# Kernel tuning notes

Hardware: AMD Instinct MI355X
Metric: run time of the kernel (lower is better)

## Reference

```python
import jax, jax.numpy as jnp
import numpy as np

HIDDEN, N_HEADS, HEAD_DIM, CACHE_LEN, BATCH = 4096, 32, 128, 512, 32


def setup_inputs() -> dict:
    key = jax.random.key(0)
    ks = jax.random.split(key, 7)
    s = 0.02
    return {
        "x": jax.random.normal(ks[0], (BATCH, 1, HIDDEN), jnp.float32),
        "k_cache": jax.random.normal(ks[1], (BATCH, N_HEADS, CACHE_LEN, HEAD_DIM), jnp.float32),
        "v_cache": jax.random.normal(ks[2], (BATCH, N_HEADS, CACHE_LEN, HEAD_DIM), jnp.float32),
        # torch nn.Linear weights: (out_features, in_features), y = x @ W.T
        "wq": jax.random.normal(ks[3], (N_HEADS * HEAD_DIM, HIDDEN), jnp.float32) * s,
        "wk": jax.random.normal(ks[4], (N_HEADS * HEAD_DIM, HIDDEN), jnp.float32) * s,
        "wv": jax.random.normal(ks[5], (N_HEADS * HEAD_DIM, HIDDEN), jnp.float32) * s,
        "wo": jax.random.normal(ks[6], (HIDDEN, N_HEADS * HEAD_DIM), jnp.float32) * s,
    }


def reference(x, k_cache, v_cache, wq, wk, wv, wo):
    bsz = x.shape[0]
    # projections: (b, 1, H*D) -> (b, n_heads, 1, head_dim)
    def proj(w):
        return (x @ w.T).reshape(bsz, 1, N_HEADS, HEAD_DIM).transpose(0, 2, 1, 3)
    q, k_new, v_new = proj(wq), proj(wk), proj(wv)
    scale = 1.0 / HEAD_DIM ** 0.5
    # cache attention: (b, h, 1, cache_len)
    cache_scores = jnp.einsum("bhqd,bhkd->bhqk", q, k_cache) * scale
    cache_probs = jax.nn.softmax(cache_scores, axis=-1)
    cache_out = jnp.einsum("bhqk,bhkd->bhqd", cache_probs, v_cache)
    # new-token attention: softmax over a single key (probs == 1), kept faithful
    new_scores = jnp.einsum("bhqd,bhkd->bhqk", q, k_new) * scale
    new_probs = jax.nn.softmax(new_scores, axis=-1)
    new_out = jnp.einsum("bhqk,bhkd->bhqd", new_probs, v_new)
    out = cache_out + new_out  # note: sum of two separately-normalized softmaxes (as in source)
    out = out.transpose(0, 2, 1, 3).reshape(bsz, 1, N_HEADS * HEAD_DIM)
    return out @ wo.T
```

## Files before the change

kernel.cpp:

```cpp
#include <hip/hip_runtime.h>
#include <hip/hip_bf16.h>

#define HIDDEN 4096
#define NHEADS 32
#define HDIM 128
#define CLEN 512
#define BATCH 32
#define KB 256

typedef float f32x4 __attribute__((ext_vector_type(4)));

__device__ __forceinline__ void proj_body(const float* __restrict__ X,
                                          const float* __restrict__ W,
                                          float* __restrict__ Y,
                                          int rowblock) {
    const int t   = threadIdx.x;
    const int l   = t & 63;
    const int wid = t >> 6;
    const int rowbase = rowblock * 8;
    const float* wp = W + (size_t)rowbase * HIDDEN + 4 * l;
    const float* xp = X + (size_t)(wid * 4) * HIDDEN + 4 * l;

    float v[32];
    #pragma unroll
    for (int j = 0; j < 32; ++j) v[j] = 0.f;

    #pragma unroll 2
    for (int kp = 0; kp < HIDDEN; kp += 256) {
        float4 wv[8], xv[4];
        #pragma unroll
        for (int r = 0; r < 8; ++r)
            wv[r] = *(const float4*)(wp + (size_t)r * HIDDEN + kp);
        #pragma unroll
        for (int b = 0; b < 4; ++b)
            xv[b] = *(const float4*)(xp + (size_t)b * HIDDEN + kp);
        #pragma unroll
        for (int r = 0; r < 8; ++r) {
            #pragma unroll
            for (int b = 0; b < 4; ++b) {
                v[r * 4 + b] += wv[r].x * xv[b].x + wv[r].y * xv[b].y +
                                wv[r].z * xv[b].z + wv[r].w * xv[b].w;
            }
        }
    }

    #pragma unroll
    for (int j = 0; j < 32; ++j) v[j] += __shfl_xor(v[j], 1);
    #pragma unroll
    for (int s = 1; s <= 5; ++s) {
        const int m = 1 << s;
        const int bit = (l >> s) & 1;
        #pragma unroll
        for (int i = 0; i < (32 >> s); ++i) {
            float t0 = __shfl_xor(v[2 * i], m);
            float t1 = __shfl_xor(v[2 * i + 1], m);
            v[i] = bit ? (v[2 * i + 1] + t1) : (v[2 * i] + t0);
        }
    }
    if (!(l & 1)) {
        const int j = l >> 1;
        const int r = j >> 2, b = j & 3;
        Y[(size_t)(wid * 4 + b) * HIDDEN + rowbase + r] = v[0];
    }
}

__global__ __launch_bounds__(512, 2) void proj_out_kernel(const float* __restrict__ X,
                                                          const float* __restrict__ W,
                                                          float* __restrict__ Y) {
    proj_body(X, W, Y, blockIdx.x);
}

__device__ __forceinline__ void proj4_body(const float* __restrict__ X,
                                           const float* __restrict__ W,
                                           float* __restrict__ Y,
                                           int rowblock) {
    const int t   = threadIdx.x;
    const int l   = t & 63;
    const int wid = t >> 6;
    const int rowbase = rowblock * 4;
    const float* wp = W + (size_t)rowbase * HIDDEN + 4 * l;
    const float* xp = X + (size_t)(wid * 8) * HIDDEN + 4 * l;

    float v[32];
    #pragma unroll
    for (int j = 0; j < 32; ++j) v[j] = 0.f;

    #pragma unroll 2
    for (int kp = 0; kp < HIDDEN; kp += 256) {
        float4 wv[4], xv[8];
        #pragma unroll
        for (int r = 0; r < 4; ++r)
            wv[r] = *(const float4*)(wp + (size_t)r * HIDDEN + kp);
        #pragma unroll
        for (int b = 0; b < 8; ++b)
            xv[b] = *(const float4*)(xp + (size_t)b * HIDDEN + kp);
        #pragma unroll
        for (int r = 0; r < 4; ++r) {
            #pragma unroll
            for (int b = 0; b < 8; ++b) {
                v[r * 8 + b] += wv[r].x * xv[b].x + wv[r].y * xv[b].y +
                                wv[r].z * xv[b].z + wv[r].w * xv[b].w;
            }
        }
    }

    #pragma unroll
    for (int j = 0; j < 32; ++j) v[j] += __shfl_xor(v[j], 1);
    #pragma unroll
    for (int s = 1; s <= 5; ++s) {
        const int m = 1 << s;
        const int bit = (l >> s) & 1;
        #pragma unroll
        for (int i = 0; i < (32 >> s); ++i) {
            float t0 = __shfl_xor(v[2 * i], m);
            float t1 = __shfl_xor(v[2 * i + 1], m);
            v[i] = bit ? (v[2 * i + 1] + t1) : (v[2 * i] + t0);
        }
    }
    if (!(l & 1)) {
        const int j = l >> 1;
        const int r = j >> 3, b = j & 7;
        Y[(size_t)(wid * 8 + b) * HIDDEN + rowbase + r] = v[0];
    }
}

__global__ __launch_bounds__(256) void proj_q_kernel(const float* __restrict__ X,
                                                     const float* __restrict__ W,
                                                     float* __restrict__ Y) {
    proj4_body(X, W, Y, blockIdx.x);
}

__device__ __forceinline__ void attn_body(const float* __restrict__ q,
                                          const float* __restrict__ kc,
                                          const float* __restrict__ vc,
                                          float* __restrict__ o_part,
                                          float* __restrict__ ms,
                                          float* __restrict__ ss,
                                          int bid) {
    const int t = threadIdx.x;
    const int w = t >> 6;
    const int l = t & 63;
    const int bh = bid >> 1;
    const int half = bid & 1;
    const int b = bh >> 5, h = bh & 31;
    const float* K = kc + (size_t)bh * CLEN * HDIM + (size_t)(half * KB + w * 64) * HDIM;
    const float* V = vc + (size_t)bh * CLEN * HDIM + (size_t)(half * KB + w * 64) * HDIM;
    const float scale = 0.088388347648318447f;
    const int d0 = 4 * (l & 31);
    const int kh = l >> 5;
    const int rot = (bid & 31) * 2;
    f32x4 q4 = *(const f32x4*)(q + (size_t)b * HIDDEN + h * HDIM + d0);

    float mloc = -INFINITY, sloc = 0.f;
    f32x4 acc = {0.f, 0.f, 0.f, 0.f};

    #pragma unroll 4
    for (int r = 0; r < 32; ++r) {
        const int k = ((2 * r + rot) & 63) + kh;
        f32x4 kv = __builtin_nontemporal_load((const f32x4*)(K + (size_t)k * HDIM + d0));
        float p = q4.x * kv.x + q4.y * kv.y + q4.z * kv.z + q4.w * kv.w;
        #pragma unroll
        for (int m = 16; m; m >>= 1) p += __shfl_xor(p, m);
        p *= scale;
        f32x4 vv = __builtin_nontemporal_load((const f32x4*)(V + (size_t)k * HDIM + d0));
        const float mn = fmaxf(mloc, p);
        const float c = __expf(mloc - mn);
        const float e = __expf(p - mn);
        sloc = sloc * c + e;
        acc = acc * c + vv * e;
        mloc = mn;
    }

    const float mo = __shfl_xor(mloc, 32);
    const float M = fmaxf(mloc, mo);
    const float wsc = __expf(mloc - M);
    float sw = sloc * wsc;
    sw += __shfl_xor(sw, 32);
    acc *= wsc;
    acc.x += __shfl_xor(acc.x, 32);
    acc.y += __shfl_xor(acc.y, 32);
    acc.z += __shfl_xor(acc.z, 32);
    acc.w += __shfl_xor(acc.w, 32);

    const int pid = bh * 8 + half * 4 + w;
    if (l < 32) *(f32x4*)(o_part + (size_t)pid * HDIM + d0) = acc;
    if (l == 0) { ms[pid] = M; ss[pid] = sw; }
}

__global__ __launch_bounds__(256, 4) void attn_projv_kernel(
        const float* __restrict__ q, const float* __restrict__ kc,
        const float* __restrict__ vc, const float* __restrict__ x,
        const float* __restrict__ wv_m, float* __restrict__ vnew,
        float* __restrict__ o_part, float* __restrict__ ms,
        float* __restrict__ ss) {
    const int bid = blockIdx.x;
    const int sel = bid % 3;
    if (sel == 2) {
        proj4_body(x, wv_m, vnew, bid / 3);
        return;
    }
    attn_body(q, kc, vc, o_part, ms, ss, (bid / 3) * 2 + sel);
}

__global__ __launch_bounds__(256) void combine_kernel(
        const float* __restrict__ o_part,
        const float* __restrict__ ms,
        const float* __restrict__ ss,
        const float* __restrict__ vnew,
        float* __restrict__ attn_out) {
    const int t = threadIdx.x;
    const int bh = blockIdx.x * 2 + (t >> 7);
    const int d = t & 127;
    float m[8];
    #pragma unroll
    for (int j = 0; j < 8; ++j) m[j] = ms[bh * 8 + j];
    float M = m[0];
    #pragma unroll
    for (int j = 1; j < 8; ++j) M = fmaxf(M, m[j]);
    float ssum = 0.f, o = 0.f;
    #pragma unroll
    for (int j = 0; j < 8; ++j) {
        const float wj = __expf(m[j] - M);
        ssum += ss[bh * 8 + j] * wj;
        o += o_part[(size_t)(bh * 8 + j) * HDIM + d] * wj;
    }
    const int b = bh >> 5, h = bh & 31;
    const size_t idx = (size_t)b * HIDDEN + h * HDIM + d;
    attn_out[idx] = o / ssum + vnew[idx];
}

extern "C" void kernel_launch(void* const* d_in, const int* in_sizes, int n_in,
                              void* d_out, int out_size, void* d_ws, size_t ws_size,
                              hipStream_t stream) {
    (void)in_sizes; (void)n_in; (void)out_size; (void)ws_size;
    const float* x  = (const float*)d_in[0];
    const float* kc = (const float*)d_in[1];
    const float* vc = (const float*)d_in[2];
    const float* wq = (const float*)d_in[3];
    const float* wv = (const float*)d_in[5];
    const float* wo = (const float*)d_in[6];
    float* out = (float*)d_out;

    float* q      = (float*)d_ws;
    float* vnew   = q + BATCH * HIDDEN;
    float* attn   = vnew + BATCH * HIDDEN;
    float* o_part = attn + BATCH * HIDDEN;
    float* ms     = o_part + 8 * BATCH * NHEADS * HDIM;
    float* ss     = ms + 8 * BATCH * NHEADS;

    proj_q_kernel<<<HIDDEN / 4, 256, 0, stream>>>(x, wq, q);
    attn_projv_kernel<<<3072, 256, 0, stream>>>(q, kc, vc, x, wv, vnew,
                                                o_part, ms, ss);
    combine_kernel<<<BATCH * NHEADS / 2, 256, 0, stream>>>(o_part, ms, ss, vnew, attn);
    proj_out_kernel<<<HIDDEN / 8, 512, 0, stream>>>(attn, wo, out);
}
```

Measured before the change: 185.3 us.

## Fuse split-softmax combine into attention block and vnew add into output projection

Each attention block now handles a whole (batch, head) with eight waves and merges their partial softmax states in shared memory, removing the separate combine kernel and the global partial buffers. The new-token value add is folded into the output projection's input load. This cuts one kernel launch and the global traffic for partials, at the cost of larger blocks, a block-wide barrier, and dropping the address rotation used to spread memory accesses.

Result: slower. 200.8 us (+8.4%).

```diff
diff --git a/kernel.cpp b/kernel.cpp
--- a/kernel.cpp
+++ b/kernel.cpp
@@ -6,69 +6,8 @@
 #define HDIM 128
 #define CLEN 512
 #define BATCH 32
-#define KB 256
 
 typedef float f32x4 __attribute__((ext_vector_type(4)));
-
-__device__ __forceinline__ void proj_body(const float* __restrict__ X,
-                                          const float* __restrict__ W,
-                                          float* __restrict__ Y,
-                                          int rowblock) {
-    const int t   = threadIdx.x;
-    const int l   = t & 63;
-    const int wid = t >> 6;
-    const int rowbase = rowblock * 8;
-    const float* wp = W + (size_t)rowbase * HIDDEN + 4 * l;
-    const float* xp = X + (size_t)(wid * 4) * HIDDEN + 4 * l;
-
-    float v[32];
-    #pragma unroll
-    for (int j = 0; j < 32; ++j) v[j] = 0.f;
-
-    #pragma unroll 2
-    for (int kp = 0; kp < HIDDEN; kp += 256) {
-        float4 wv[8], xv[4];
-        #pragma unroll
-        for (int r = 0; r < 8; ++r)
-            wv[r] = *(const float4*)(wp + (size_t)r * HIDDEN + kp);
-        #pragma unroll
-        for (int b = 0; b < 4; ++b)
-            xv[b] = *(const float4*)(xp + (size_t)b * HIDDEN + kp);
-        #pragma unroll
-        for (int r = 0; r < 8; ++r) {
-            #pragma unroll
-            for (int b = 0; b < 4; ++b) {
-                v[r * 4 + b] += wv[r].x * xv[b].x + wv[r].y * xv[b].y +
-                                wv[r].z * xv[b].z + wv[r].w * xv[b].w;
-            }
-        }
-    }
-
-    #pragma unroll
-    for (int j = 0; j < 32; ++j) v[j] += __shfl_xor(v[j], 1);
-    #pragma unroll
-    for (int s = 1; s <= 5; ++s) {
-        const int m = 1 << s;
-        const int bit = (l >> s) & 1;
-        #pragma unroll
-        for (int i = 0; i < (32 >> s); ++i) {
-            float t0 = __shfl_xor(v[2 * i], m);
-            float t1 = __shfl_xor(v[2 * i + 1], m);
-            v[i] = bit ? (v[2 * i + 1] + t1) : (v[2 * i] + t0);
-        }
-    }
-    if (!(l & 1)) {
-        const int j = l >> 1;
-        const int r = j >> 2, b = j & 3;
-        Y[(size_t)(wid * 4 + b) * HIDDEN + rowbase + r] = v[0];
-    }
-}
-
-__global__ __launch_bounds__(512, 2) void proj_out_kernel(const float* __restrict__ X,
-                                                          const float* __restrict__ W,
-                                                          float* __restrict__ Y) {
-    proj_body(X, W, Y, blockIdx.x);
-}
 
 __device__ __forceinline__ void proj4_body(const float* __restrict__ X,
                                            const float* __restrict__ W,
@@ -130,25 +69,76 @@
     proj4_body(X, W, Y, blockIdx.x);
 }
 
+__device__ __forceinline__ void proj8_body(const float* __restrict__ X,
+                                           const float* __restrict__ W,
+                                           float* __restrict__ Y,
+                                           int rowblock) {
+    const int t   = threadIdx.x;
+    const int l   = t & 63;
+    const int wid = t >> 6;
+    const int rowbase = rowblock * 8;
+    const float* wp = W + (size_t)rowbase * HIDDEN + 4 * l;
+    const float* xp = X + (size_t)(wid * 4) * HIDDEN + 4 * l;
+
+    float v[32];
+    #pragma unroll
+    for (int j = 0; j < 32; ++j) v[j] = 0.f;
+
+    #pragma unroll 2
+    for (int kp = 0; kp < HIDDEN; kp += 256) {
+        float4 wv[8], xv[4];
+        #pragma unroll
+        for (int r = 0; r < 8; ++r)
+            wv[r] = *(const float4*)(wp + (size_t)r * HIDDEN + kp);
+        #pragma unroll
+        for (int b = 0; b < 4; ++b)
+            xv[b] = *(const float4*)(xp + (size_t)b * HIDDEN + kp);
+        #pragma unroll
+        for (int r = 0; r < 8; ++r) {
+            #pragma unroll
+            for (int b = 0; b < 4; ++b) {
+                v[r * 4 + b] += wv[r].x * xv[b].x + wv[r].y * xv[b].y +
+                                wv[r].z * xv[b].z + wv[r].w * xv[b].w;
+            }
+        }
+    }
+
+    #pragma unroll
+    for (int j = 0; j < 32; ++j) v[j] += __shfl_xor(v[j], 1);
+    #pragma unroll
+    for (int s = 1; s <= 5; ++s) {
+        const int m = 1 << s;
+        const int bit = (l >> s) & 1;
+        #pragma unroll
+        for (int i = 0; i < (32 >> s); ++i) {
+            float t0 = __shfl_xor(v[2 * i], m);
+            float t1 = __shfl_xor(v[2 * i + 1], m);
+            v[i] = bit ? (v[2 * i + 1] + t1) : (v[2 * i] + t0);
+        }
+    }
+    if (!(l & 1)) {
+        const int j = l >> 1;
+        const int r = j >> 2, b = j & 3;
+        Y[(size_t)(wid * 4 + b) * HIDDEN + rowbase + r] = v[0];
+    }
+}
+
 __device__ __forceinline__ void attn_body(const float* __restrict__ q,
                                           const float* __restrict__ kc,
                                           const float* __restrict__ vc,
-                                          float* __restrict__ o_part,
-                                          float* __restrict__ ms,
-                                          float* __restrict__ ss,
-                                          int bid) {
+                                          float* __restrict__ attn_out,
+                                          int bh) {
+    __shared__ float lo[8][HDIM];
+    __shared__ float lm[8], lsw[8];
     const int t = threadIdx.x;
     const int w = t >> 6;
     const int l = t & 63;
-    const int bh = bid >> 1;
-    const int half = bid & 1;
     const int b = bh >> 5, h = bh & 31;
-    const float* K = kc + (size_t)bh * CLEN * HDIM + (size_t)(half * KB + w * 64) * HDIM;
-    const float* V = vc + (size_t)bh * CLEN * HDIM + (size_t)(half * KB + w * 64) * HDIM;
+    const float* K = kc + (size_t)bh * CLEN * HDIM;
+    const float* V = vc + (size_t)bh * CLEN * HDIM;
     const float scale = 0.088388347648318447f;
     const int d0 = 4 * (l & 31);
     const int kh = l >> 5;
-    const int rot = (bid & 31) * 2;
     f32x4 q4 = *(const f32x4*)(q + (size_t)b * HIDDEN + h * HDIM + d0);
 
     float mloc = -INFINITY, sloc = 0.f;
@@ -156,7 +146,7 @@
 
     #pragma unroll 4
     for (int r = 0; r < 32; ++r) {
-        const int k = ((2 * r + rot) & 63) + kh;
+        const int k = r * 16 + w * 2 + kh;
         f32x4 kv = __builtin_nontemporal_load((const f32x4*)(K + (size_t)k * HDIM + d0));
         float p = q4.x * kv.x + q4.y * kv.y + q4.z * kv.z + q4.w * kv.w;
         #pragma unroll
@@ -182,51 +172,91 @@
     acc.z += __shfl_xor(acc.z, 32);
     acc.w += __shfl_xor(acc.w, 32);
 
-    const int pid = bh * 8 + half * 4 + w;
-    if (l < 32) *(f32x4*)(o_part + (size_t)pid * HDIM + d0) = acc;
-    if (l == 0) { ms[pid] = M; ss[pid] = sw; }
-}
-
-__global__ __launch_bounds__(256, 4) void attn_projv_kernel(
+    if (l < 32) *(f32x4*)(&lo[w][d0]) = acc;
+    if (l == 0) { lm[w] = M; lsw[w] = sw; }
+    __syncthreads();
+    if (t < HDIM) {
+        float M8 = lm[0];
+        #pragma unroll
+        for (int j = 1; j < 8; ++j) M8 = fmaxf(M8, lm[j]);
+        float o = 0.f, ssum = 0.f;
+        #pragma unroll
+        for (int j = 0; j < 8; ++j) {
+            const float ej = __expf(lm[j] - M8);
+            o += lo[j][t] * ej;
+            ssum += lsw[j] * ej;
+        }
+        attn_out[(size_t)b * HIDDEN + h * HDIM + t] = o / ssum;
+    }
+}
+
+__global__ __launch_bounds__(512, 4) void attn_projv_kernel(
         const float* __restrict__ q, const float* __restrict__ kc,
         const float* __restrict__ vc, const float* __restrict__ x,
         const float* __restrict__ wv_m, float* __restrict__ vnew,
-        float* __restrict__ o_part, float* __restrict__ ms,
-        float* __restrict__ ss) {
+        float* __restrict__ attn_out) {
     const int bid = blockIdx.x;
     const int sel = bid % 3;
     if (sel == 2) {
-        proj4_body(x, wv_m, vnew, bid / 3);
+        proj8_body(x, wv_m, vnew, bid / 3);
         return;
     }
-    attn_body(q, kc, vc, o_part, ms, ss, (bid / 3) * 2 + sel);
-}
-
-__global__ __launch_bounds__(256) void combine_kernel(
-        const float* __restrict__ o_part,
-        const float* __restrict__ ms,
-        const float* __restrict__ ss,
-        const float* __restrict__ vnew,
-        float* __restrict__ attn_out) {
-    const int t = threadIdx.x;
-    const int bh = blockIdx.x * 2 + (t >> 7);
-    const int d = t & 127;
-    float m[8];
-    #pragma unroll
-    for (int j = 0; j < 8; ++j) m[j] = ms[bh * 8 + j];
-    float M = m[0];
-    #pragma unroll
-    for (int j = 1; j < 8; ++j) M = fmaxf(M, m[j]);
-    float ssum = 0.f, o = 0.f;
-    #pragma unroll
-    for (int j = 0; j < 8; ++j) {
-        const float wj = __expf(m[j] - M);
-        ssum += ss[bh * 8 + j] * wj;
-        o += o_part[(size_t)(bh * 8 + j) * HDIM + d] * wj;
-    }
-    const int b = bh >> 5, h = bh & 31;
-    const size_t idx = (size_t)b * HIDDEN + h * HDIM + d;
-    attn_out[idx] = o / ssum + vnew[idx];
+    attn_body(q, kc, vc, attn_out, (bid / 3) * 2 + sel);
+}
+
+__global__ __launch_bounds__(512, 2) void proj_out_kernel(
+        const float* __restrict__ Xa, const float* __restrict__ Xb,
+        const float* __restrict__ W, float* __restrict__ Y) {
+    const int t   = threadIdx.x;
+    const int l   = t & 63;
+    const int wid = t >> 6;
+    const int rowbase = blockIdx.x * 8;
+    const float* wp = W + (size_t)rowbase * HIDDEN + 4 * l;
+    const int col0 = 4 * l;
+
+    float v[32];
+    #pragma unroll
+    for (int j = 0; j < 32; ++j) v[j] = 0.f;
+
+    #pragma unroll 2
+    for (int kp = 0; kp < HIDDEN; kp += 256) {
+        f32x4 wv[8], xv[4];
+        #pragma unroll
+        for (int r = 0; r < 8; ++r)
+            wv[r] = *(const f32x4*)(wp + (size_t)r * HIDDEN + kp);
+        #pragma unroll
+        for (int b = 0; b < 4; ++b) {
+            const size_t off = (size_t)(wid * 4 + b) * HIDDEN + col0 + kp;
+            xv[b] = *(const f32x4*)(Xa + off) + *(const f32x4*)(Xb + off);
+        }
+        #pragma unroll
+        for (int r = 0; r < 8; ++r) {
+            #pragma unroll
+            for (int b = 0; b < 4; ++b) {
+                v[r * 4 + b] += wv[r].x * xv[b].x + wv[r].y * xv[b].y +
+                                wv[r].z * xv[b].z + wv[r].w * xv[b].w;
+            }
+        }
+    }
+
+    #pragma unroll
+    for (int j = 0; j < 32; ++j) v[j] += __shfl_xor(v[j], 1);
+    #pragma unroll
+    for (int s = 1; s <= 5; ++s) {
+        const int m = 1 << s;
+        const int bit = (l >> s) & 1;
+        #pragma unroll
+        for (int i = 0; i < (32 >> s); ++i) {
+            float t0 = __shfl_xor(v[2 * i], m);
+            float t1 = __shfl_xor(v[2 * i + 1], m);
+            v[i] = bit ? (v[2 * i + 1] + t1) : (v[2 * i] + t0);
+        }
+    }
+    if (!(l & 1)) {
+        const int j = l >> 1;
+        const int r = j >> 2, b = j & 3;
+        Y[(size_t)(wid * 4 + b) * HIDDEN + rowbase + r] = v[0];
+    }
 }
 
 extern "C" void kernel_launch(void* const* d_in, const int* in_sizes, int n_in,
@@ -241,16 +271,11 @@
     const float* wo = (const float*)d_in[6];
     float* out = (float*)d_out;
 
-    float* q      = (float*)d_ws;
-    float* vnew   = q + BATCH * HIDDEN;
-    float* attn   = vnew + BATCH * HIDDEN;
-    float* o_part = attn + BATCH * HIDDEN;
-    float* ms     = o_part + 8 * BATCH * NHEADS * HDIM;
-    float* ss     = ms + 8 * BATCH * NHEADS;
+    float* q    = (float*)d_ws;
+    float* vnew = q + BATCH * HIDDEN;
+    float* attn = vnew + BATCH * HIDDEN;
 
     proj_q_kernel<<<HIDDEN / 4, 256, 0, stream>>>(x, wq, q);
-    attn_projv_kernel<<<3072, 256, 0, stream>>>(q, kc, vc, x, wv, vnew,
-                                                o_part, ms, ss);
-    combine_kernel<<<BATCH * NHEADS / 2, 256, 0, stream>>>(o_part, ms, ss, vnew, attn);
-    proj_out_kernel<<<HIDDEN / 8, 512, 0, stream>>>(attn, wo, out);
-}
+    attn_projv_kernel<<<1536, 512, 0, stream>>>(q, kc, vc, x, wv, vnew, attn);
+    proj_out_kernel<<<HIDDEN / 8, 512, 0, stream>>>(attn, vnew, wo, out);
+}
```
